# Optimization experiments

Hardware: AMD Instinct MI355X
Metric: run time of the kernel (lower is better)

Reference implementation:

```python
import jax, jax.numpy as jnp
import numpy as np

INPUT_DIM = 1024
NUM_HEADS = 16


def setup_inputs() -> dict:
    key = jax.random.key(0)
    k1, k2, k3, k4, k5, k6, k7, k8 = jax.random.split(key, 8)
    bs, seq, dm = 2, 2048, INPUT_DIM
    scale = 1.0 / np.sqrt(dm)
    return {
        "input": jax.random.normal(k1, (bs, seq, dm), dtype=jnp.float32),
        "mask": jax.random.randint(k2, (bs, seq), 0, 2, dtype=jnp.int32),
        "Wq": jax.random.normal(k3, (dm, dm), dtype=jnp.float32) * scale,
        "bq": jax.random.normal(k4, (dm,), dtype=jnp.float32) * 0.01,
        "Wk": jax.random.normal(k5, (dm, dm), dtype=jnp.float32) * scale,
        "bk": jax.random.normal(k6, (dm,), dtype=jnp.float32) * 0.01,
        "Wv": jax.random.normal(k7, (dm, dm), dtype=jnp.float32) * scale,
        "bv": jax.random.normal(k8, (dm,), dtype=jnp.float32) * 0.01,
    }


def reference(input, mask, Wq, bq, Wk, bk, Wv, bv):
    bs, seq, dm = input.shape
    h = NUM_HEADS
    d = dm // h
    # projections: x @ W^T + b (torch Linear convention)
    Q = (input @ Wq.T + bq).reshape(bs, seq, h, d).transpose(0, 2, 1, 3)
    K = (input @ Wk.T + bk).reshape(bs, seq, h, d).transpose(0, 2, 1, 3)
    V = (input @ Wv.T + bv).reshape(bs, seq, h, d).transpose(0, 2, 1, 3)
    # raw scores [bs, h, seq, seq]
    scores = jnp.einsum("bhqd,bhkd->bhqk", Q, K)
    m = mask.astype(jnp.float32).reshape(bs, 1, 1, seq)
    # mask_logits is applied BEFORE the 1/sqrt(d) scaling, as in source
    scores = scores * m + (1.0 - m) * (-1e30)
    scores = scores * (1.0 / np.sqrt(d))
    attn = jax.nn.softmax(scores, axis=-1)  # dropout = identity at eval
    out = jnp.einsum("bhqk,bhkd->bhqd", attn, V)
    return out.transpose(0, 2, 1, 3).reshape(bs, seq, dm)
```

## Files before the change

### kernel.cpp

```cpp
#include <hip/hip_runtime.h>
#include <stdint.h>
#include <stddef.h>

#define SEQ 2048
#define DM  1024
#define NH  16
#define BS  2

typedef __attribute__((ext_vector_type(8)))  __bf16 bf16x8;
typedef __attribute__((ext_vector_type(4)))  __bf16 bf16x4;
typedef __attribute__((ext_vector_type(4)))  float  floatx4;
typedef __attribute__((ext_vector_type(16))) float  floatx16;
typedef __attribute__((ext_vector_type(4)))  unsigned int uintx4;
typedef __attribute__((ext_vector_type(4)))  unsigned short ushortx4;

#if __has_builtin(__builtin_amdgcn_exp2f)
#define EXP2(x) __builtin_amdgcn_exp2f(x)
#else
#define EXP2(x) __expf((x) * 0.6931471805599453f)
#endif

#define QSCALE 0.18033688011112042f

#define GLDS(g, s) __builtin_amdgcn_global_load_lds( \
    (const __attribute__((address_space(1))) void*)(g), \
    (__attribute__((address_space(3))) void*)(s), 16, 0, 0)

__device__ inline unsigned short f2bf(float f) {
  union { float f; unsigned int u; } a; a.f = f;
  unsigned int u = a.u;
  return (unsigned short)((u + 0x7fffu + ((u >> 16) & 1u)) >> 16);
}

__device__ inline bf16x8 ldb8(const unsigned short* p) { return *(const bf16x8*)p; }

__global__ __launch_bounds__(256) void prep(
    const float* __restrict__ x, const float* __restrict__ wq,
    const float* __restrict__ wk, const float* __restrict__ wv,
    const int* __restrict__ mask,
    unsigned short* __restrict__ Xb, unsigned short* __restrict__ Wb,
    unsigned short* __restrict__ mb01) {
  const int bid = blockIdx.x, t = threadIdx.x;
  if (bid < 7168) {
    const float* src; unsigned short* dst; int base;
    if (bid < 4096)      { src = x;  dst = Xb;            base = bid; }
    else if (bid < 5120) { src = wq; dst = Wb;            base = bid - 4096; }
    else if (bid < 6144) { src = wk; dst = Wb + 1048576;  base = bid - 5120; }
    else                 { src = wv; dst = Wb + 2097152;  base = bid - 6144; }
    const int i = base * 256 + t;
    floatx4 v = ((const floatx4*)src)[i];
    ushortx4 o;
    o.x = f2bf(v.x); o.y = f2bf(v.y); o.z = f2bf(v.z); o.w = f2bf(v.w);
    ((ushortx4*)dst)[i] = o;
  } else {
    const int i = (bid - 7168) * 256 + t;
    mb01[i] = mask[i] ? 0x3F80 : 0;
  }
}

__global__ __launch_bounds__(256, 3) void gemm_qkv(
    const unsigned short* __restrict__ Xb, const unsigned short* __restrict__ Wb,
    const float* __restrict__ bq, const float* __restrict__ bk, const float* __restrict__ bv,
    const int* __restrict__ mask,
    unsigned short* __restrict__ Qb, unsigned short* __restrict__ Kb,
    unsigned short* __restrict__ Vt)
{
  __shared__ alignas(16) unsigned short LB[16384];
  const int t = threadIdx.x;
  const int w = t >> 6, l = t & 63;
  const int lm = l & 15, lq = l >> 4;
  const int z = blockIdx.z;
  const size_t m0 = (size_t)blockIdx.y * 128;
  const size_t n0 = (size_t)blockIdx.x * 128;
  const unsigned short* W = Wb + (size_t)z * (1024 * 1024);
  const float* bias = (z == 0) ? bq : ((z == 1) ? bk : bv);
  const float sc = (z == 0) ? QSCALE : 1.0f;

  const int c0 = t, c1 = 256 + t;
  const int row0 = c0 >> 2, row1 = c1 >> 2;
  const int kq0 = (c0 & 3) ^ ((row0 >> 1) & 3);
  const int kq1 = (c1 & 3) ^ ((row1 >> 1) & 3);
  const unsigned short* gA0 = Xb + (m0 + row0) * 1024 + kq0 * 8;
  const unsigned short* gA1 = Xb + (m0 + row1) * 1024 + kq1 * 8;
  const unsigned short* gB0 = W + (n0 + row0) * 1024 + kq0 * 8;
  const unsigned short* gB1 = W + (n0 + row1) * 1024 + kq1 * 8;
  const int la0 = (0 * 256 + w * 64) * 8;
  const int la1 = (1 * 256 + w * 64) * 8;

  const int wr = (w >> 1) * 64, wc = (w & 1) * 64;
  const int sw = (lq ^ ((lm >> 1) & 3)) * 8;
  floatx4 acc[4][4] = {};

  GLDS(gA0, LB + la0);
  GLDS(gA1, LB + la1);
  GLDS(gB0, LB + 8192 + la0);
  GLDS(gB1, LB + 8192 + la1);
  __syncthreads();

  for (int it = 0; it < 32; ++it) {
    const int cur = it & 1;
    if (it < 31) {
      const int kn = (it + 1) * 32;
      const int nb = (cur ^ 1) * 4096;
      GLDS(gA0 + kn, LB + nb + la0);
      GLDS(gA1 + kn, LB + nb + la1);
      GLDS(gB0 + kn, LB + 8192 + nb + la0);
      GLDS(gB1 + kn, LB + 8192 + nb + la1);
    }
    const unsigned short* Ab = LB + cur * 4096;
    const unsigned short* Bb = LB + 8192 + cur * 4096;
    bf16x8 af[4], bfr[4];
#pragma unroll
    for (int i = 0; i < 4; i++) af[i] = ldb8(Ab + (wr + i * 16 + lm) * 32 + sw);
#pragma unroll
    for (int j = 0; j < 4; j++) bfr[j] = ldb8(Bb + (wc + j * 16 + lm) * 32 + sw);
#pragma unroll
    for (int i = 0; i < 4; i++)
#pragma unroll
      for (int j = 0; j < 4; j++)
        acc[i][j] = __builtin_amdgcn_mfma_f32_16x16x32_bf16(af[i], bfr[j], acc[i][j], 0, 0, 0);
    __syncthreads();
  }

  if (z < 2) {
    unsigned short* dst = (z == 0) ? Qb : Kb;
#pragma unroll
    for (int j = 0; j < 4; j++) {
      const int ncol = (int)n0 + wc + j * 16 + lm;
      const float bval = bias[ncol];
#pragma unroll
      for (int i = 0; i < 4; i++)
#pragma unroll
        for (int r = 0; r < 4; r++) {
          const int mrow = (int)m0 + wr + i * 16 + lq * 4 + r;
          dst[(size_t)mrow * 1024 + ncol] = f2bf((acc[i][j][r] + bval) * sc);
        }
    }
  } else {
    float mk[4][4];
#pragma unroll
    for (int i = 0; i < 4; i++)
#pragma unroll
      for (int r = 0; r < 4; r++)
        mk[i][r] = (float)mask[(int)m0 + wr + i * 16 + lq * 4 + r];
#pragma unroll
    for (int j = 0; j < 4; j++) {
      const int nl = wc + j * 16 + lm;
      const float bval = bias[(int)n0 + nl];
#pragma unroll
      for (int i = 0; i < 4; i++)
#pragma unroll
        for (int r = 0; r < 4; r++) {
          const int ml = wr + i * 16 + lq * 4 + r;
          LB[nl * 128 + ((((ml >> 3) ^ (nl & 15)) * 8) | (ml & 7))] =
              f2bf((acc[i][j][r] + bval) * mk[i][r]);
        }
    }
    __syncthreads();
    const int nl = t >> 1, hf = t & 1;
    const int ncol = (int)n0 + nl;
    const int hh = ncol >> 6, dc = ncol & 63;
    const int bb = (int)(m0 >> 11);
    const int s0c = ((int)m0 & 2047) + hf * 64;
    unsigned short* dstp = Vt + (size_t)((bb * 16 + hh) * 64 + dc) * SEQ + s0c;
#pragma unroll
    for (int u = 0; u < 8; ++u) {
      const int phys = (hf * 8 + u) ^ (nl & 15);
      *(uintx4*)(dstp + u * 8) = *(const uintx4*)(LB + nl * 128 + phys * 8);
    }
  }
}

__global__ __launch_bounds__(256, 2) void attn(
    const unsigned short* __restrict__ Qb, const unsigned short* __restrict__ Kb,
    const unsigned short* __restrict__ Vt, const unsigned short* __restrict__ mb01,
    float* __restrict__ out)
{
  __shared__ alignas(16) unsigned short Klds[2][4096];
  __shared__ alignas(16) unsigned short Vlds[3][4096];
  __shared__ alignas(16) unsigned short Plds[2][4][2048];
  __shared__ alignas(16) unsigned short Mb[2048];

  const int t = threadIdx.x, w = t >> 6, l = t & 63;
  const int ln = l & 31, h = l >> 5;
  const int bid = blockIdx.x;
  const int pp = bid & 31;
  const int b = pp >> 4, head = pp & 15;
  const int q0w = (bid >> 5) * 128 + w * 32;
  const int hoff = head * 64;

  const int sr = l >> 3;
  const int gc = (l & 7) ^ sr;
  const unsigned short* gK[2]; const unsigned short* gV[2];
#pragma unroll
  for (int s2 = 0; s2 < 2; ++s2) {
    const int row = w * 16 + s2 * 8 + sr;
    gK[s2] = Kb + (size_t)(b * SEQ + row) * DM + hoff + gc * 8;
    gV[s2] = Vt + (size_t)((b * NH + head) * 64 + row) * SEQ + gc * 8;
  }

#pragma unroll
  for (int s2 = 0; s2 < 2; ++s2) {
    GLDS(gK[s2],                   &Klds[0][(w * 128 + s2 * 64) * 8]);
    GLDS(gK[s2] + (size_t)64 * DM, &Klds[1][(w * 128 + s2 * 64) * 8]);
    GLDS(gV[s2],                   &Vlds[0][(w * 128 + s2 * 64) * 8]);
  }

  ((uintx4*)Mb)[t] = ((const uintx4*)(mb01 + b * SEQ))[t];

  const unsigned short* Qbase = Qb + (size_t)(b * SEQ + q0w + ln) * DM + hoff + h * 8;
  bf16x8 qf[4];
#pragma unroll
  for (int c = 0; c < 4; ++c) qf[c] = ldb8(Qbase + c * 16);

  const int cc = (ln >> 1) & 3, hb = h ^ (ln & 1);
  int xoff[4];
#pragma unroll
  for (int c = 0; c < 4; ++c) xoff[c] = (c ^ cc) * 16 + hb * 8;

  floatx16 oacc[2] = {};
  floatx16 tacc = {};

  __syncthreads();

  floatx16 scur[2] = {};
  {
    const unsigned short* Kc = &Klds[0][ln * 64];
#pragma unroll
    for (int c = 0; c < 4; ++c) {
      scur[0] = __builtin_amdgcn_mfma_f32_32x32x16_bf16(ldb8(Kc + xoff[c]),        qf[c], scur[0], 0, 0, 0);
      scur[1] = __builtin_amdgcn_mfma_f32_32x32x16_bf16(ldb8(Kc + 2048 + xoff[c]), qf[c], scur[1], 0, 0, 0);
    }
  }
  __syncthreads();

  for (int kt = 0; kt < 32; ++kt) {
    if (kt < 30) {
#pragma unroll
      for (int s2 = 0; s2 < 2; ++s2)
        GLDS(gK[s2] + (size_t)(kt + 2) * 64 * DM, &Klds[kt & 1][(w * 128 + s2 * 64) * 8]);
    }
    if (kt < 31) {
#pragma unroll
      for (int s2 = 0; s2 < 2; ++s2)
        GLDS(gV[s2] + (kt + 1) * 64, &Vlds[(kt + 1) % 3][(w * 128 + s2 * 64) * 8]);
    }

    floatx16 snext[2] = {};
    if (kt < 31) {
      const unsigned short* Kc = &Klds[(kt + 1) & 1][ln * 64];
#pragma unroll
      for (int c = 0; c < 4; ++c) {
        snext[0] = __builtin_amdgcn_mfma_f32_32x32x16_bf16(ldb8(Kc + xoff[c]),        qf[c], snext[0], 0, 0, 0);
        snext[1] = __builtin_amdgcn_mfma_f32_32x32x16_bf16(ldb8(Kc + 2048 + xoff[c]), qf[c], snext[1], 0, 0, 0);
      }
    }

    {
      unsigned short* Pw = &Plds[kt & 1][w][ln * 64];
#pragma unroll
      for (int kb = 0; kb < 2; ++kb)
#pragma unroll
        for (int g = 0; g < 4; ++g) {
          bf16x4 pk;
#pragma unroll
          for (int r = 0; r < 4; ++r) pk[r] = (__bf16)EXP2(scur[kb][g * 4 + r]);
          *(bf16x4*)(Pw + ((4 * kb + g) ^ (ln & 7)) * 8 + h * 4) = pk;
        }
    }

    if (kt > 0) {
      const unsigned short* Pw = &Plds[(kt - 1) & 1][w][ln * 64];
      const unsigned short* Vc = &Vlds[(kt - 1) % 3][ln * 64];
      bf16x8 pf[4];
#pragma unroll
      for (int c = 0; c < 4; ++c) pf[c] = ldb8(Pw + xoff[c]);
      const int k0 = (kt - 1) * 64;
#pragma unroll
      for (int c = 0; c < 4; ++c) {
        const bf16x8 mfr = ldb8(Mb + k0 + c * 16 + h * 8);
        tacc = __builtin_amdgcn_mfma_f32_32x32x16_bf16(pf[c], mfr, tacc, 0, 0, 0);
      }
#pragma unroll
      for (int c = 0; c < 4; ++c) {
        oacc[0] = __builtin_amdgcn_mfma_f32_32x32x16_bf16(pf[c], ldb8(Vc + xoff[c]),        oacc[0], 0, 0, 0);
        oacc[1] = __builtin_amdgcn_mfma_f32_32x32x16_bf16(pf[c], ldb8(Vc + 2048 + xoff[c]), oacc[1], 0, 0, 0);
      }
    }

    scur[0] = snext[0]; scur[1] = snext[1];
    __syncthreads();
  }

  {
    const unsigned short* Pw = &Plds[1][w][ln * 64];
    const unsigned short* Vc = &Vlds[1][ln * 64];
    bf16x8 pf[4];
#pragma unroll
    for (int c = 0; c < 4; ++c) pf[c] = ldb8(Pw + xoff[c]);
    const int k0 = 31 * 64;
#pragma unroll
    for (int c = 0; c < 4; ++c) {
      const bf16x8 mfr = ldb8(Mb + k0 + c * 16 + h * 8);
      tacc = __builtin_amdgcn_mfma_f32_32x32x16_bf16(pf[c], mfr, tacc, 0, 0, 0);
    }
#pragma unroll
    for (int c = 0; c < 4; ++c) {
      oacc[0] = __builtin_amdgcn_mfma_f32_32x32x16_bf16(pf[c], ldb8(Vc + xoff[c]),        oacc[0], 0, 0, 0);
      oacc[1] = __builtin_amdgcn_mfma_f32_32x32x16_bf16(pf[c], ldb8(Vc + 2048 + xoff[c]), oacc[1], 0, 0, 0);
    }
  }

  float* obase = out + (size_t)(b * SEQ + q0w) * DM + hoff;
#pragma unroll
  for (int r = 0; r < 16; ++r) {
    const int rq = (r & 3) + 8 * (r >> 2) + 4 * h;
    const float iv = __builtin_amdgcn_rcpf(tacc[r]);
    obase[(size_t)rq * DM + ln]      = oacc[0][r] * iv;
    obase[(size_t)rq * DM + 32 + ln] = oacc[1][r] * iv;
  }
}

extern "C" void kernel_launch(void* const* d_in, const int* in_sizes, int n_in,
                              void* d_out, int out_size, void* d_ws, size_t ws_size,
                              hipStream_t stream) {
  const float* x   = (const float*)d_in[0];
  const int*   msk = (const int*)d_in[1];
  const float* Wq  = (const float*)d_in[2];
  const float* bq  = (const float*)d_in[3];
  const float* Wk  = (const float*)d_in[4];
  const float* bk  = (const float*)d_in[5];
  const float* Wv  = (const float*)d_in[6];
  const float* bv  = (const float*)d_in[7];
  float* out = (float*)d_out;

  unsigned short* ws = (unsigned short*)d_ws;
  unsigned short* Xb = ws;
  unsigned short* Wb = Xb + (size_t)4096 * 1024;
  unsigned short* Qb = Wb + (size_t)3 * 1024 * 1024;
  unsigned short* Kb = Qb + (size_t)4096 * 1024;
  unsigned short* Vt = Kb + (size_t)4096 * 1024;
  unsigned short* mb01 = Vt + (size_t)4096 * 1024;

  prep<<<7184, 256, 0, stream>>>(x, Wq, Wk, Wv, msk, Xb, Wb, mb01);

  gemm_qkv<<<dim3(8, 32, 3), 256, 0, stream>>>(Xb, Wb, bq, bk, bv, msk, Qb, Kb, Vt);

  attn<<<512, 256, 0, stream>>>(Qb, Kb, Vt, mb01, out);
}
```

Measured before the change: 174.5 us.

## Keep softmax P fragments in registers with cross-lane shuffles instead of LDS

Removes the LDS staging buffer for the exponentiated score tile P. Each lane now packs its bf16 probabilities into registers, and the A-operand layout for the PV and row-sum MFMAs is rebuilt with a 32-lane xor shuffle. Score accumulators are double-buffered in register arrays, and the loop is unrolled by 2 so the buffer indices stay static. This trades LDS writes and reads, plus some LDS capacity, for extra VGPR pressure and shuffle instructions, which could hurt occupancy at launch_bounds(256,2).

```diff
diff --git a/kernel.cpp b/kernel.cpp
--- a/kernel.cpp
+++ b/kernel.cpp
@@ -178,7 +178,6 @@
 {
   __shared__ alignas(16) unsigned short Klds[2][4096];
   __shared__ alignas(16) unsigned short Vlds[3][4096];
-  __shared__ alignas(16) unsigned short Plds[2][4][2048];
   __shared__ alignas(16) unsigned short Mb[2048];
 
   const int t = threadIdx.x, w = t >> 6, l = t & 63;
@@ -220,25 +219,31 @@
 
   floatx16 oacc[2] = {};
   floatx16 tacc = {};
+  floatx16 sbuf[2][2];
+  unsigned long long pkb[2][8];
 
   __syncthreads();
 
-  floatx16 scur[2] = {};
+  sbuf[0][0] = (floatx16){};
+  sbuf[0][1] = (floatx16){};
   {
     const unsigned short* Kc = &Klds[0][ln * 64];
 #pragma unroll
     for (int c = 0; c < 4; ++c) {
-      scur[0] = __builtin_amdgcn_mfma_f32_32x32x16_bf16(ldb8(Kc + xoff[c]),        qf[c], scur[0], 0, 0, 0);
-      scur[1] = __builtin_amdgcn_mfma_f32_32x32x16_bf16(ldb8(Kc + 2048 + xoff[c]), qf[c], scur[1], 0, 0, 0);
+      sbuf[0][0] = __builtin_amdgcn_mfma_f32_32x32x16_bf16(ldb8(Kc + xoff[c]),        qf[c], sbuf[0][0], 0, 0, 0);
+      sbuf[0][1] = __builtin_amdgcn_mfma_f32_32x32x16_bf16(ldb8(Kc + 2048 + xoff[c]), qf[c], sbuf[0][1], 0, 0, 0);
     }
   }
   __syncthreads();
 
+#pragma unroll 2
   for (int kt = 0; kt < 32; ++kt) {
+    const int pcur = kt & 1, pprv = (kt + 1) & 1;
+
     if (kt < 30) {
 #pragma unroll
       for (int s2 = 0; s2 < 2; ++s2)
-        GLDS(gK[s2] + (size_t)(kt + 2) * 64 * DM, &Klds[kt & 1][(w * 128 + s2 * 64) * 8]);
+        GLDS(gK[s2] + (size_t)(kt + 2) * 64 * DM, &Klds[pcur][(w * 128 + s2 * 64) * 8]);
     }
     if (kt < 31) {
 #pragma unroll
@@ -246,68 +251,69 @@
         GLDS(gV[s2] + (kt + 1) * 64, &Vlds[(kt + 1) % 3][(w * 128 + s2 * 64) * 8]);
     }
 
-    floatx16 snext[2] = {};
     if (kt < 31) {
-      const unsigned short* Kc = &Klds[(kt + 1) & 1][ln * 64];
+      floatx16 sn0 = {}, sn1 = {};
+      const unsigned short* Kc = &Klds[pprv][ln * 64];
 #pragma unroll
       for (int c = 0; c < 4; ++c) {
-        snext[0] = __builtin_amdgcn_mfma_f32_32x32x16_bf16(ldb8(Kc + xoff[c]),        qf[c], snext[0], 0, 0, 0);
-        snext[1] = __builtin_amdgcn_mfma_f32_32x32x16_bf16(ldb8(Kc + 2048 + xoff[c]), qf[c], snext[1], 0, 0, 0);
+        sn0 = __builtin_amdgcn_mfma_f32_32x32x16_bf16(ldb8(Kc + xoff[c]),        qf[c], sn0, 0, 0, 0);
+        sn1 = __builtin_amdgcn_mfma_f32_32x32x16_bf16(ldb8(Kc + 2048 + xoff[c]), qf[c], sn1, 0, 0, 0);
       }
-    }
-
-    {
-      unsigned short* Pw = &Plds[kt & 1][w][ln * 64];
-#pragma unroll
-      for (int kb = 0; kb < 2; ++kb)
-#pragma unroll
-        for (int g = 0; g < 4; ++g) {
-          bf16x4 pk;
-#pragma unroll
-          for (int r = 0; r < 4; ++r) pk[r] = (__bf16)EXP2(scur[kb][g * 4 + r]);
-          *(bf16x4*)(Pw + ((4 * kb + g) ^ (ln & 7)) * 8 + h * 4) = pk;
-        }
-    }
+      sbuf[pprv][0] = sn0; sbuf[pprv][1] = sn1;
+    }
+
+#pragma unroll
+    for (int kb = 0; kb < 2; ++kb)
+#pragma unroll
+      for (int g = 0; g < 4; ++g) {
+        union { bf16x4 v; unsigned long long u; } pu;
+#pragma unroll
+        for (int r = 0; r < 4; ++r) pu.v[r] = (__bf16)EXP2(sbuf[pcur][kb][g * 4 + r]);
+        pkb[pcur][kb * 4 + g] = pu.u;
+      }
 
     if (kt > 0) {
-      const unsigned short* Pw = &Plds[(kt - 1) & 1][w][ln * 64];
       const unsigned short* Vc = &Vlds[(kt - 1) % 3][ln * 64];
-      bf16x8 pf[4];
-#pragma unroll
-      for (int c = 0; c < 4; ++c) pf[c] = ldb8(Pw + xoff[c]);
       const int k0 = (kt - 1) * 64;
 #pragma unroll
       for (int c = 0; c < 4; ++c) {
+        const int kb = c >> 1, ge = (c & 1) * 2, go = ge + 1;
+        const unsigned long long snd = h ? pkb[pprv][kb * 4 + ge] : pkb[pprv][kb * 4 + go];
+        const unsigned long long rcv =
+            (unsigned long long)__shfl_xor((long long)snd, 32, 64);
+        union { unsigned long long u[2]; bf16x8 v; } fu;
+        fu.u[0] = h ? rcv : pkb[pprv][kb * 4 + ge];
+        fu.u[1] = h ? pkb[pprv][kb * 4 + go] : rcv;
+        const bf16x8 pf = fu.v;
+
         const bf16x8 mfr = ldb8(Mb + k0 + c * 16 + h * 8);
-        tacc = __builtin_amdgcn_mfma_f32_32x32x16_bf16(pf[c], mfr, tacc, 0, 0, 0);
+        tacc = __builtin_amdgcn_mfma_f32_32x32x16_bf16(pf, mfr, tacc, 0, 0, 0);
+        oacc[0] = __builtin_amdgcn_mfma_f32_32x32x16_bf16(pf, ldb8(Vc + xoff[c]),        oacc[0], 0, 0, 0);
+        oacc[1] = __builtin_amdgcn_mfma_f32_32x32x16_bf16(pf, ldb8(Vc + 2048 + xoff[c]), oacc[1], 0, 0, 0);
       }
-#pragma unroll
-      for (int c = 0; c < 4; ++c) {
-        oacc[0] = __builtin_amdgcn_mfma_f32_32x32x16_bf16(pf[c], ldb8(Vc + xoff[c]),        oacc[0], 0, 0, 0);
-        oacc[1] = __builtin_amdgcn_mfma_f32_32x32x16_bf16(pf[c], ldb8(Vc + 2048 + xoff[c]), oacc[1], 0, 0, 0);
-      }
-    }
-
-    scur[0] = snext[0]; scur[1] = snext[1];
+    }
+
     __syncthreads();
   }
 
   {
-    const unsigned short* Pw = &Plds[1][w][ln * 64];
     const unsigned short* Vc = &Vlds[1][ln * 64];
-    bf16x8 pf[4];
-#pragma unroll
-    for (int c = 0; c < 4; ++c) pf[c] = ldb8(Pw + xoff[c]);
     const int k0 = 31 * 64;
 #pragma unroll
     for (int c = 0; c < 4; ++c) {
+      const int kb = c >> 1, ge = (c & 1) * 2, go = ge + 1;
+      const unsigned long long snd = h ? pkb[1][kb * 4 + ge] : pkb[1][kb * 4 + go];
+      const unsigned long long rcv =
+          (unsigned long long)__shfl_xor((long long)snd, 32, 64);
+      union { unsigned long long u[2]; bf16x8 v; } fu;
+      fu.u[0] = h ? rcv : pkb[1][kb * 4 + ge];
+      fu.u[1] = h ? pkb[1][kb * 4 + go] : rcv;
+      const bf16x8 pf = fu.v;
+
       const bf16x8 mfr = ldb8(Mb + k0 + c * 16 + h * 8);
-      tacc = __builtin_amdgcn_mfma_f32_32x32x16_bf16(pf[c], mfr, tacc, 0, 0, 0);
-    }
-#pragma unroll
-    for (int c = 0; c < 4; ++c) {
-      oacc[0] = __builtin_amdgcn_mfma_f32_32x32x16_bf16(pf[c], ldb8(Vc + xoff[c]),        oacc[0], 0, 0, 0);
-      oacc[1] = __builtin_amdgcn_mfma_f32_32x32x16_bf16(pf[c], ldb8(Vc + 2048 + xoff[c]), oacc[1], 0, 0, 0);
+      tacc = __builtin_amdgcn_mfma_f32_32x32x16_bf16(pf, mfr, tacc, 0, 0, 0);
+      oacc[0] = __builtin_amdgcn_mfma_f32_32x32x16_bf16(pf, ldb8(Vc + xoff[c]),        oacc[0], 0, 0, 0);
+      oacc[1] = __builtin_amdgcn_mfma_f32_32x32x16_bf16(pf, ldb8(Vc + 2048 + xoff[c]), oacc[1], 0, 0, 0);
     }
   }
 
```

New measurement: 214.8 us. 1.23x slower.
